# Performance work log

Measured on AMD Instinct MI355X. Metric: run time of the kernel, lower is better.

Reference implementation:

```python
import jax, jax.numpy as jnp
import numpy as np

N_NODES = 100000
N_EDGES = 1600000
D_INPUT = 128
D_HIDDEN = 16
N_HEADS = 8
NCLASSES = 40
N_GRAPHS = 64
ALPHA = 0.2  # LeakyReLU negative slope
INIT = 0.01  # GAT_param_init uniform range


def setup_inputs() -> dict:
    key = jax.random.key(0)
    ks = jax.random.split(key, 7)
    x = jax.random.normal(ks[0], (N_NODES, D_INPUT), dtype=jnp.float32)
    edge_idx = jax.random.randint(ks[1], (2, N_EDGES), 0, N_NODES, dtype=jnp.int64)
    batch = jnp.sort(jax.random.randint(ks[2], (N_NODES,), 0, N_GRAPHS, dtype=jnp.int64))
    # layer1: d_input -> n_heads * d_hidden, concat aggregate
    W1 = jax.random.uniform(ks[3], (D_INPUT, N_HEADS * D_HIDDEN), dtype=jnp.float32, minval=-INIT, maxval=INIT)
    a1 = jax.random.uniform(ks[4], (N_HEADS, 2 * D_HIDDEN), dtype=jnp.float32, minval=-INIT, maxval=INIT)
    # layer2: n_heads*d_hidden -> nclasses, 1 head, mean aggregate
    W2 = jax.random.uniform(ks[5], (N_HEADS * D_HIDDEN, NCLASSES), dtype=jnp.float32, minval=-INIT, maxval=INIT)
    a2 = jax.random.uniform(ks[6], (1, 2 * NCLASSES), dtype=jnp.float32, minval=-INIT, maxval=INIT)
    return {"x": x, "W1": W1, "a1": a1, "W2": W2, "a2": a2, "edge_idx": edge_idx, "batch": batch}


def _gat_layer(x, W, a, n_heads, d_out, src, dst, aggregate):
    # x: [N, d_in]; W: [d_in, H*D]; a: [H, 2*D]
    n = x.shape[0]
    Wh = (x @ W).reshape(n, n_heads, d_out)                  # [N, H, D]
    e_src = jnp.einsum('nhd,hd->nh', Wh, a[:, :d_out])       # [N, H]
    e_dst = jnp.einsum('nhd,hd->nh', Wh, a[:, d_out:])       # [N, H]
    e = jax.nn.leaky_relu(e_src[src] + e_dst[dst], ALPHA)    # [E, H]
    # segment softmax over edges sharing the same destination node
    m = jax.ops.segment_max(e, dst, num_segments=n)          # [N, H]
    m = jnp.where(jnp.isfinite(m), m, 0.0)                   # nodes w/o in-edges
    ex = jnp.exp(e - m[dst])
    s = jax.ops.segment_sum(ex, dst, num_segments=n)
    att = ex / (s[dst] + 1e-16)                              # [E, H]
    # weighted scatter-aggregate of neighbor features
    out = jax.ops.segment_sum(att[:, :, None] * Wh[src], dst, num_segments=n)  # [N, H, D]
    if aggregate == 'concat':
        return out.reshape(n, n_heads * d_out)
    return out.mean(axis=1)


def reference(x, W1, a1, W2, a2, edge_idx, batch):
    # eval mode: F.dropout(training=False) is identity
    src, dst = edge_idx[0], edge_idx[1]
    h1 = _gat_layer(x, W1, a1, N_HEADS, D_HIDDEN, src, dst, 'concat')
    h1 = jax.nn.elu(h1)
    h2 = _gat_layer(h1, W2, a2, 1, NCLASSES, src, dst, 'mean')   # [N, nclasses]
    # global_mean_pool over graph ids
    sums = jax.ops.segment_sum(h2, batch, num_segments=N_GRAPHS)
    cnt = jax.ops.segment_sum(jnp.ones((h2.shape[0],), h2.dtype), batch, num_segments=N_GRAPHS)
    return sums / jnp.maximum(cnt, 1.0)[:, None]
```

## Files before the change

### kernel.cpp

```cpp
#include <hip/hip_runtime.h>
#include <hip/hip_bf16.h>

typedef unsigned short u16;
typedef unsigned int   u32;

static constexpr int NN = 100000;
static constexpr int NE = 1600000;
static constexpr int NG = 64;

static constexpr int BSH   = 8;
static constexpr int NBUCK = 391;
static constexpr int BCAP  = 5120;
static constexpr int PB    = 8;

__device__ __forceinline__ u32 bf16pair(float a, float b) {
  u32 ua = __builtin_bit_cast(u32, a), ub = __builtin_bit_cast(u32, b);
  ua = (ua + 0x7FFFu + ((ua >> 16) & 1u)) >> 16;
  ub = (ub + 0x7FFFu + ((ub >> 16) & 1u)) >> 16;
  return ua | (ub << 16);
}
__device__ __forceinline__ float bflo(u32 u) { return __builtin_bit_cast(float, u << 16); }
__device__ __forceinline__ float bfhi(u32 u) { return __builtin_bit_cast(float, u & 0xFFFF0000u); }

__global__ __launch_bounds__(256) void k_gemm1(
    const float* __restrict__ x, const float* __restrict__ W1,
    const float* __restrict__ a1,
    u16* __restrict__ Wh1b, float* __restrict__ es1, float* __restrict__ ed1)
{
  __shared__ float xs[64][36];
  __shared__ float ws[32][128];
  const int t = threadIdx.x;
  const int rowBase = blockIdx.x * 64;
  const int r0 = (t >> 4) * 4;
  const int c0 = (t & 15) * 8;
  float acc[4][8];
#pragma unroll
  for (int r = 0; r < 4; ++r)
#pragma unroll
    for (int c = 0; c < 8; ++c) acc[r][c] = 0.f;

  for (int k0 = 0; k0 < 128; k0 += 32) {
#pragma unroll
    for (int p = 0; p < 2; ++p) {
      int rr = (t >> 3) + p * 32;
      int cc = (t & 7) * 4;
      int grow = rowBase + rr;
      float4 v = make_float4(0.f, 0.f, 0.f, 0.f);
      if (grow < NN) v = *(const float4*)(&x[(size_t)grow * 128 + k0 + cc]);
      *(float4*)(&xs[rr][cc]) = v;
    }
#pragma unroll
    for (int p = 0; p < 4; ++p) {
      int idx = (p * 256 + t) * 4;
      int kk = idx >> 7, cc = idx & 127;
      *(float4*)(&ws[kk][cc]) = *(const float4*)(&W1[(size_t)(k0 + kk) * 128 + cc]);
    }
    __syncthreads();
#pragma unroll
    for (int k = 0; k < 32; ++k) {
      float a[4], b[8];
#pragma unroll
      for (int r = 0; r < 4; ++r) a[r] = xs[r0 + r][k];
      *(float4*)&b[0] = *(float4*)&ws[k][c0];
      *(float4*)&b[4] = *(float4*)&ws[k][c0 + 4];
#pragma unroll
      for (int r = 0; r < 4; ++r)
#pragma unroll
        for (int c = 0; c < 8; ++c) acc[r][c] = fmaf(a[r], b[c], acc[r][c]);
    }
    __syncthreads();
  }
  const int h = (t & 15) >> 1;
  const int dbase = (t & 1) * 8;
  float a1s[8], a1d[8];
#pragma unroll
  for (int j = 0; j < 8; ++j) {
    a1s[j] = a1[h * 32 + dbase + j];
    a1d[j] = a1[h * 32 + 16 + dbase + j];
  }
#pragma unroll
  for (int r = 0; r < 4; ++r) {
    int grow = rowBase + r0 + r;
    float pes = 0.f, ped = 0.f;
#pragma unroll
    for (int j = 0; j < 8; ++j) {
      pes = fmaf(acc[r][j], a1s[j], pes);
      ped = fmaf(acc[r][j], a1d[j], ped);
    }
    pes += __shfl_xor(pes, 1);
    ped += __shfl_xor(ped, 1);
    if (grow < NN) {
      u32 p0 = bf16pair(acc[r][0], acc[r][1]);
      u32 p1 = bf16pair(acc[r][2], acc[r][3]);
      u32 p2 = bf16pair(acc[r][4], acc[r][5]);
      u32 p3 = bf16pair(acc[r][6], acc[r][7]);
      *(uint4*)(Wh1b + (size_t)grow * 128 + c0) = make_uint4(p0, p1, p2, p3);
      if ((t & 1) == 0) { es1[grow * 8 + h] = pes; ed1[grow * 8 + h] = ped; }
    }
  }
}

__global__ __launch_bounds__(256) void k_gemm2(
    const float* __restrict__ h1, const float* __restrict__ W2,
    const float* __restrict__ a2,
    u16* __restrict__ Wh2b, float* __restrict__ es2, float* __restrict__ ed2)
{
  __shared__ float hs[128][36];
  __shared__ float w2s[32][40];
  const int t = threadIdx.x;
  const int rowBase = blockIdx.x * 128;
  const int cg = t & 3;
  const int rs = t >> 2;
  float acc[2][10];
#pragma unroll
  for (int r = 0; r < 2; ++r)
#pragma unroll
    for (int j = 0; j < 10; ++j) acc[r][j] = 0.f;

  for (int k0 = 0; k0 < 128; k0 += 32) {
#pragma unroll
    for (int p = 0; p < 4; ++p) {
      int idx = (p * 256 + t) * 4;
      int rr = idx >> 5, cc = idx & 31;
      int grow = rowBase + rr;
      float4 v = make_float4(0.f, 0.f, 0.f, 0.f);
      if (grow < NN) v = *(const float4*)(&h1[(size_t)grow * 128 + k0 + cc]);
      *(float4*)(&hs[rr][cc]) = v;
    }
#pragma unroll
    for (int p = 0; p < 5; ++p) {
      int idx = p * 256 + t;
      int kk = idx / 40, cc = idx % 40;
      w2s[kk][cc] = W2[(size_t)(k0 + kk) * 40 + cc];
    }
    __syncthreads();
#pragma unroll
    for (int k = 0; k < 32; ++k) {
      float a0 = hs[rs][k], a1v = hs[rs + 64][k];
#pragma unroll
      for (int j = 0; j < 10; ++j) {
        float b = w2s[k][cg * 10 + j];
        acc[0][j] = fmaf(a0, b, acc[0][j]);
        acc[1][j] = fmaf(a1v, b, acc[1][j]);
      }
    }
    __syncthreads();
  }
  float a2s[10], a2d[10];
#pragma unroll
  for (int j = 0; j < 10; ++j) {
    a2s[j] = a2[cg * 10 + j];
    a2d[j] = a2[40 + cg * 10 + j];
  }
#pragma unroll
  for (int rr = 0; rr < 2; ++rr) {
    int grow = rowBase + rs + rr * 64;
    float pes = 0.f, ped = 0.f;
#pragma unroll
    for (int j = 0; j < 10; ++j) {
      float v = acc[rr][j];
      pes = fmaf(v, a2s[j], pes);
      ped = fmaf(v, a2d[j], ped);
    }
    if (grow < NN) {
      u32* dst = (u32*)(Wh2b + (size_t)grow * 48 + cg * 10);
      dst[0] = bf16pair(acc[rr][0], acc[rr][1]);
      dst[1] = bf16pair(acc[rr][2], acc[rr][3]);
      dst[2] = bf16pair(acc[rr][4], acc[rr][5]);
      dst[3] = bf16pair(acc[rr][6], acc[rr][7]);
      dst[4] = bf16pair(acc[rr][8], acc[rr][9]);
    }
    pes += __shfl_xor(pes, 1); pes += __shfl_xor(pes, 2);
    ped += __shfl_xor(ped, 1); ped += __shfl_xor(ped, 2);
    if (cg == 0 && grow < NN) { es2[grow] = pes; ed2[grow] = ped; }
  }
}

__global__ void k_initcur(int* __restrict__ cur) {
  int t = blockIdx.x * 256 + threadIdx.x;
  if (t < NBUCK) cur[t] = t * BCAP;
}

__global__ __launch_bounds__(256) void k_bin(
    const int* __restrict__ src, const int* __restrict__ dst,
    int* __restrict__ cur, u32* __restrict__ ebuf)
{
  __shared__ int lcnt[512];
  __shared__ int goff[NBUCK];
  __shared__ u32 bin[4096];
  const int t = threadIdx.x;
  const int e0 = blockIdx.x * 4096;

  lcnt[t] = 0; lcnt[t + 256] = 0;
  __syncthreads();

  u32 ent[16]; short bb[16], lp[16];
#pragma unroll
  for (int i = 0; i < 16; ++i) {
    int e = e0 + i * 256 + t;
    if (e < NE) {
      int s = src[e], d = dst[e];
      int b = d >> BSH;
      ent[i] = (u32)s | ((u32)(d & 255) << 20);
      bb[i] = (short)b;
      lp[i] = (short)atomicAdd(&lcnt[b], 1);
    } else bb[i] = -1;
  }
  __syncthreads();
  for (int d = 1; d < 512; d <<= 1) {
    int v0 = (t >= d) ? lcnt[t - d] : 0;
    int v1 = (t + 256 >= d) ? lcnt[t + 256 - d] : 0;
    __syncthreads();
    lcnt[t] += v0; lcnt[t + 256] += v1;
    __syncthreads();
  }
  for (int b = t; b < NBUCK; b += 256) {
    int excl = b ? lcnt[b - 1] : 0;
    int cnt = lcnt[b] - excl;
    if (cnt) goff[b] = atomicAdd(&cur[b], cnt);
  }
#pragma unroll
  for (int i = 0; i < 16; ++i) {
    if (bb[i] >= 0) {
      int excl = bb[i] ? lcnt[bb[i] - 1] : 0;
      bin[excl + lp[i]] = ent[i];
    }
  }
  __syncthreads();
  const int total = lcnt[NBUCK - 1];
  for (int i = t; i < total; i += 256) {
    int lo = 0, hi = NBUCK - 1;
    while (lo < hi) { int mid = (lo + hi) >> 1; if (lcnt[mid] > i) hi = mid; else lo = mid + 1; }
    int excl = lo ? lcnt[lo - 1] : 0;
    int g = goff[lo] + (i - excl);
    if (g < (lo + 1) * BCAP) ebuf[g] = bin[i];
  }
}

__global__ __launch_bounds__(256) void k_sort(
    const int* __restrict__ cur, u32* __restrict__ ebuf,
    int* __restrict__ offs, int* __restrict__ deg)
{
  __shared__ u32 ein[BCAP];
  __shared__ u32 eout[BCAP];
  __shared__ int nd[256];
  __shared__ int ncur[256];
  const int t = threadIdx.x;
  const int b = blockIdx.x;
  const int base = b * BCAP;
  int cnt = cur[b] - base;
  if (cnt > BCAP) cnt = BCAP;
  const int nloc = min(256, NN - (b << BSH));

  for (int i = t; i < cnt; i += 256) ein[i] = ebuf[base + i];
  nd[t] = 0;
  __syncthreads();
  for (int i = t; i < cnt; i += 256) atomicAdd(&nd[ein[i] >> 20], 1);
  __syncthreads();
  const int myCnt = nd[t];
  for (int d = 1; d < 256; d <<= 1) {
    int v = (t >= d) ? nd[t - d] : 0;
    __syncthreads();
    nd[t] += v;
    __syncthreads();
  }
  const int excl = t ? nd[t - 1] : 0;
  ncur[t] = excl;
  if (t < nloc) {
    int node = (b << BSH) + t;
    offs[node] = base + excl;
    deg[node]  = myCnt;
  }
  __syncthreads();
  for (int i = t; i < cnt; i += 256) {
    u32 v = ein[i];
    int pos = atomicAdd(&ncur[v >> 20], 1);
    eout[pos] = v & 0xFFFFFu;
  }
  __syncthreads();
  for (int i = t; i < cnt; i += 256) ebuf[base + i] = eout[i];
}

__global__ __launch_bounds__(256) void k_agg1(
    const u16* __restrict__ Wh1b, const float* __restrict__ es1, const float* __restrict__ ed1,
    const int* __restrict__ offs, const int* __restrict__ deg, const int* __restrict__ csr,
    float* __restrict__ h1)
{
  const int wid = threadIdx.x >> 6;
  const int lane = threadIdx.x & 63;
  const int n = blockIdx.x * 4 + wid;
  if (n >= NN) return;
  const int s0 = offs[n];
  const int nE = deg[n];
  const int g = lane >> 4;
  const int db = lane & 15;
  const int h = db >> 1;
  const float edv = ed1[n * 8 + h];

  float acc[8];
#pragma unroll
  for (int i = 0; i < 8; ++i) acc[i] = 0.f;
  float ssum = 0.f;

  for (int c0 = 0; c0 < nE; c0 += 8) {
    const int j0 = c0 + g;
    const int j1 = c0 + 4 + g;
    const int sA = csr[s0 + (j0 < nE ? j0 : 0)];
    const int sB = csr[s0 + (j1 < nE ? j1 : 0)];
    float zA = es1[sA * 8 + h] + edv;
    float zB = es1[sB * 8 + h] + edv;
    zA = (zA > 0.f) ? zA : 0.2f * zA;
    zB = (zB > 0.f) ? zB : 0.2f * zB;
    if (j0 < nE) {
      const uint4 raw = *(const uint4*)(Wh1b + (size_t)sA * 128 + db * 8);
      const float w = __expf(zA);
      ssum += w;
      acc[0] = fmaf(w, bflo(raw.x), acc[0]);
      acc[1] = fmaf(w, bfhi(raw.x), acc[1]);
      acc[2] = fmaf(w, bflo(raw.y), acc[2]);
      acc[3] = fmaf(w, bfhi(raw.y), acc[3]);
      acc[4] = fmaf(w, bflo(raw.z), acc[4]);
      acc[5] = fmaf(w, bfhi(raw.z), acc[5]);
      acc[6] = fmaf(w, bflo(raw.w), acc[6]);
      acc[7] = fmaf(w, bfhi(raw.w), acc[7]);
    }
    if (j1 < nE) {
      const uint4 raw = *(const uint4*)(Wh1b + (size_t)sB * 128 + db * 8);
      const float w = __expf(zB);
      ssum += w;
      acc[0] = fmaf(w, bflo(raw.x), acc[0]);
      acc[1] = fmaf(w, bfhi(raw.x), acc[1]);
      acc[2] = fmaf(w, bflo(raw.y), acc[2]);
      acc[3] = fmaf(w, bfhi(raw.y), acc[3]);
      acc[4] = fmaf(w, bflo(raw.z), acc[4]);
      acc[5] = fmaf(w, bfhi(raw.z), acc[5]);
      acc[6] = fmaf(w, bflo(raw.w), acc[6]);
      acc[7] = fmaf(w, bfhi(raw.w), acc[7]);
    }
  }
#pragma unroll
  for (int i = 0; i < 8; ++i) {
    acc[i] += __shfl_xor(acc[i], 16);
    acc[i] += __shfl_xor(acc[i], 32);
  }
  ssum += __shfl_xor(ssum, 16);
  ssum += __shfl_xor(ssum, 32);

  if (g == 0) {
    float inv = 1.f / (ssum + 1e-16f);
    float o[8];
#pragma unroll
    for (int i = 0; i < 8; ++i) {
      float v = acc[i] * inv;
      o[i] = (v > 0.f) ? v : expm1f(v);
    }
    float* dst = h1 + (size_t)n * 128 + db * 8;
    *(float4*)(dst)     = make_float4(o[0], o[1], o[2], o[3]);
    *(float4*)(dst + 4) = make_float4(o[4], o[5], o[6], o[7]);
  }
}

__global__ __launch_bounds__(256) void k_agg2(
    const u16* __restrict__ Wh2b, const float* __restrict__ es2, const float* __restrict__ ed2,
    const int* __restrict__ offs, const int* __restrict__ deg, const int* __restrict__ csr,
    float* __restrict__ h2)
{
  __shared__ float red[4][64][9];
  const int wid = threadIdx.x >> 6;
  const int lane = threadIdx.x & 63;
  const int n = blockIdx.x * 4 + wid;
  if (n >= NN) return;
  const int s0 = offs[n];
  const int nE = deg[n];
  const float edv = ed2[n];
  const int e5 = lane / 5, r5 = lane - e5 * 5;
  const bool act = lane < 60;

  float acc[8];
#pragma unroll
  for (int i = 0; i < 8; ++i) acc[i] = 0.f;
  float ssum = 0.f;

  for (int c0 = 0; c0 < nE; c0 += 24) {
    const int j0 = c0 + e5;
    const int j1 = c0 + 12 + e5;
    const int sA = csr[s0 + (j0 < nE ? j0 : 0)];
    const int sB = csr[s0 + (j1 < nE ? j1 : 0)];
    float zA = es2[sA] + edv;
    float zB = es2[sB] + edv;
    zA = (zA > 0.f) ? zA : 0.2f * zA;
    zB = (zB > 0.f) ? zB : 0.2f * zB;
    if (act && j0 < nE) {
      const uint4 raw = *(const uint4*)(Wh2b + (size_t)sA * 48 + r5 * 8);
      const float w = __expf(zA);
      ssum += w;
      acc[0] = fmaf(w, bflo(raw.x), acc[0]);
      acc[1] = fmaf(w, bfhi(raw.x), acc[1]);
      acc[2] = fmaf(w, bflo(raw.y), acc[2]);
      acc[3] = fmaf(w, bfhi(raw.y), acc[3]);
      acc[4] = fmaf(w, bflo(raw.z), acc[4]);
      acc[5] = fmaf(w, bfhi(raw.z), acc[5]);
      acc[6] = fmaf(w, bflo(raw.w), acc[6]);
      acc[7] = fmaf(w, bfhi(raw.w), acc[7]);
    }
    if (act && j1 < nE) {
      const uint4 raw = *(const uint4*)(Wh2b + (size_t)sB * 48 + r5 * 8);
      const float w = __expf(zB);
      ssum += w;
      acc[0] = fmaf(w, bflo(raw.x), acc[0]);
      acc[1] = fmaf(w, bfhi(raw.x), acc[1]);
      acc[2] = fmaf(w, bflo(raw.y), acc[2]);
      acc[3] = fmaf(w, bfhi(raw.y), acc[3]);
      acc[4] = fmaf(w, bflo(raw.z), acc[4]);
      acc[5] = fmaf(w, bfhi(raw.z), acc[5]);
      acc[6] = fmaf(w, bflo(raw.w), acc[6]);
      acc[7] = fmaf(w, bfhi(raw.w), acc[7]);
    }
  }
#pragma unroll
  for (int i = 0; i < 8; ++i) red[wid][lane][i] = acc[i];
  red[wid][lane][8] = ssum;
  __builtin_amdgcn_wave_barrier();
  if (lane < 40) {
    int slot = lane >> 3, i = lane & 7;
    float a = 0.f, sm = 0.f;
#pragma unroll
    for (int g = 0; g < 12; ++g) {
      a  += red[wid][g * 5 + slot][i];
      sm += red[wid][g * 5][8];
    }
    h2[(size_t)n * 40 + lane] = a / (sm + 1e-16f);
  }
}

__global__ void k_gbounds(const int* __restrict__ batch, int* __restrict__ gstart) {
  int g = threadIdx.x;
  if (g > NG) return;
  int lo = 0, hi = NN;
  while (lo < hi) { int mid = (lo + hi) >> 1; if (batch[mid] < g) lo = mid + 1; else hi = mid; }
  gstart[g] = lo;
}

__global__ __launch_bounds__(256) void k_pool1(
    const float* __restrict__ h2, const int* __restrict__ gstart,
    float* __restrict__ partial)
{
  __shared__ float lds[25][10][4];
  const int g = blockIdx.x >> 3;
  const int p = blockIdx.x & 7;
  const int t = threadIdx.x;
  const int s0 = gstart[g], s1 = gstart[g + 1];
  const int len = s1 - s0;
  const int chunk = (len + PB - 1) / PB;
  const int start = s0 + p * chunk;
  const int end = min(start + chunk, s1);
  const int slot = t / 10, q = t - slot * 10;
  float4 acc = make_float4(0.f, 0.f, 0.f, 0.f);
  if (slot < 25) {
    for (int n = start + slot; n < end; n += 25) {
      const float4 v = *(const float4*)(&h2[(size_t)n * 40 + q * 4]);
      acc.x += v.x; acc.y += v.y; acc.z += v.z; acc.w += v.w;
    }
    lds[slot][q][0] = acc.x; lds[slot][q][1] = acc.y;
    lds[slot][q][2] = acc.z; lds[slot][q][3] = acc.w;
  }
  __syncthreads();
  if (t < 40) {
    const int qq = t >> 2, e = t & 3;
    float s = 0.f;
#pragma unroll
    for (int sl = 0; sl < 25; ++sl) s += lds[sl][qq][e];
    partial[(size_t)blockIdx.x * 40 + t] = s;
  }
}

__global__ void k_pool2(const float* __restrict__ partial, const int* __restrict__ gstart,
                        float* __restrict__ out)
{
  const int g = blockIdx.x;
  const int d = threadIdx.x;
  if (d >= 40) return;
  float s = 0.f;
#pragma unroll
  for (int p = 0; p < PB; ++p) s += partial[(size_t)(g * PB + p) * 40 + d];
  int cnt = gstart[g + 1] - gstart[g];
  if (cnt < 1) cnt = 1;
  out[g * 40 + d] = s / (float)cnt;
}

extern "C" void kernel_launch(void* const* d_in, const int* in_sizes, int n_in,
                              void* d_out, int out_size, void* d_ws, size_t ws_size,
                              hipStream_t stream)
{
  const float* x   = (const float*)d_in[0];
  const float* W1  = (const float*)d_in[1];
  const float* a1  = (const float*)d_in[2];
  const float* W2  = (const float*)d_in[3];
  const float* a2  = (const float*)d_in[4];
  const int* eidx  = (const int*)d_in[5];
  const int* batch = (const int*)d_in[6];
  float* out = (float*)d_out;

  char* ws = (char*)d_ws;
  u16*   Wh1b = (u16*)(ws + 0);
  u16*   Wh2b = (u16*)(ws + 0);
  float* h2   = (float*)(ws + 9600000);
  float* h1   = (float*)(ws + 25600000);
  float* es1  = (float*)(ws + 76800000);
  float* ed1  = (float*)(ws + 80000000);
  float* es2  = (float*)(ws + 83200000);
  float* ed2  = (float*)(ws + 83600000);
  u32*   ebuf = (u32*)(ws + 84000000);
  int*   offs = (int*)(ws + 92007680);
  int*   deg  = (int*)(ws + 92407680);
  int*   cur  = (int*)(ws + 92807680);
  int*   gstart = (int*)(ws + 92809728);
  float* partial = (float*)(ws + 92810240);

  const int* esrc = eidx;
  const int* edst = eidx + NE;

  k_initcur<<<2, 256, 0, stream>>>(cur);
  k_gbounds<<<1, 128, 0, stream>>>(batch, gstart);
  k_gemm1<<<(NN + 63) / 64, 256, 0, stream>>>(x, W1, a1, Wh1b, es1, ed1);
  k_bin<<<(NE + 4095) / 4096, 256, 0, stream>>>(esrc, edst, cur, ebuf);
  k_sort<<<NBUCK, 256, 0, stream>>>(cur, ebuf, offs, deg);
  k_agg1<<<(NN + 3) / 4, 256, 0, stream>>>(Wh1b, es1, ed1, offs, deg, (const int*)ebuf, h1);
  k_gemm2<<<(NN + 127) / 128, 256, 0, stream>>>(h1, W2, a2, Wh2b, es2, ed2);
  k_agg2<<<(NN + 3) / 4, 256, 0, stream>>>(Wh2b, es2, ed2, offs, deg, (const int*)ebuf, h2);
  k_pool1<<<NG * PB, 256, 0, stream>>>(h2, gstart, partial);
  k_pool2<<<NG, 64, 0, stream>>>(partial, gstart, out);
}
```

Before: 284.0 us.

## Fuse front kernels, store h1 in bf16, use packed FMA in aggregations

Merges edge binning, the first GEMM and the graph-bound search into one launch with a shared-memory union, and replaces the cursor-init kernel with a memset by making bucket cursors relative. Layer-1 output is now written as bf16 and converted back to fp32 inside the second GEMM, halving that intermediate traffic. Both aggregation kernels switch to v_pk_fma_f32 inline asm on float2 accumulators to halve FMA issue count. The bf16 h1 adds rounding error into layer 2, and the inline asm constrains compiler scheduling.

```diff
diff --git a/kernel.cpp b/kernel.cpp
--- a/kernel.cpp
+++ b/kernel.cpp
@@ -3,6 +3,7 @@
 
 typedef unsigned short u16;
 typedef unsigned int   u32;
+typedef float f32x2 __attribute__((ext_vector_type(2)));
 
 static constexpr int NN = 100000;
 static constexpr int NE = 1600000;
@@ -12,6 +13,7 @@
 static constexpr int NBUCK = 391;
 static constexpr int BCAP  = 5120;
 static constexpr int PB    = 8;
+static constexpr int NB_G1 = (NN + 63) / 64;
 
 __device__ __forceinline__ u32 bf16pair(float a, float b) {
   u32 ua = __builtin_bit_cast(u32, a), ub = __builtin_bit_cast(u32, b);
@@ -22,15 +24,84 @@
 __device__ __forceinline__ float bflo(u32 u) { return __builtin_bit_cast(float, u << 16); }
 __device__ __forceinline__ float bfhi(u32 u) { return __builtin_bit_cast(float, u & 0xFFFF0000u); }
 
-__global__ __launch_bounds__(256) void k_gemm1(
-    const float* __restrict__ x, const float* __restrict__ W1,
-    const float* __restrict__ a1,
-    u16* __restrict__ Wh1b, float* __restrict__ es1, float* __restrict__ ed1)
-{
-  __shared__ float xs[64][36];
-  __shared__ float ws[32][128];
+__device__ __forceinline__ void pkfma(f32x2& a, f32x2 w2, u32 u) {
+  f32x2 v;
+  v.x = bflo(u); v.y = bfhi(u);
+  asm("v_pk_fma_f32 %0, %1, %2, %0" : "+v"(a) : "v"(w2), "v"(v));
+}
+
+__global__ __launch_bounds__(256) void k_front(
+    const float* __restrict__ x, const float* __restrict__ W1, const float* __restrict__ a1,
+    const int* __restrict__ esrc, const int* __restrict__ edst, const int* __restrict__ batch,
+    u16* __restrict__ Wh1b, float* __restrict__ es1, float* __restrict__ ed1,
+    int* __restrict__ cur, u32* __restrict__ ebuf, int* __restrict__ gstart)
+{
+  __shared__ union U {
+    struct { float xs[64][36]; float ws[32][128]; } g;
+    struct { int lcnt[512]; int goff[NBUCK]; u32 bin[4096]; } b;
+  } sm;
+  const int bid = blockIdx.x;
   const int t = threadIdx.x;
-  const int rowBase = blockIdx.x * 64;
+
+  if (bid < NBUCK) {
+    const int e0 = bid * 4096;
+    sm.b.lcnt[t] = 0; sm.b.lcnt[t + 256] = 0;
+    __syncthreads();
+    u32 ent[16]; short bb[16], lp[16];
+#pragma unroll
+    for (int i = 0; i < 16; ++i) {
+      int e = e0 + i * 256 + t;
+      if (e < NE) {
+        int s = esrc[e], d = edst[e];
+        int b = d >> BSH;
+        ent[i] = (u32)s | ((u32)(d & 255) << 20);
+        bb[i] = (short)b;
+        lp[i] = (short)atomicAdd(&sm.b.lcnt[b], 1);
+      } else bb[i] = -1;
+    }
+    __syncthreads();
+    for (int d = 1; d < 512; d <<= 1) {
+      int v0 = (t >= d) ? sm.b.lcnt[t - d] : 0;
+      int v1 = (t + 256 >= d) ? sm.b.lcnt[t + 256 - d] : 0;
+      __syncthreads();
+      sm.b.lcnt[t] += v0; sm.b.lcnt[t + 256] += v1;
+      __syncthreads();
+    }
+    for (int b = t; b < NBUCK; b += 256) {
+      int excl = b ? sm.b.lcnt[b - 1] : 0;
+      int cnt = sm.b.lcnt[b] - excl;
+      if (cnt) sm.b.goff[b] = b * BCAP + atomicAdd(&cur[b], cnt);
+    }
+#pragma unroll
+    for (int i = 0; i < 16; ++i) {
+      if (bb[i] >= 0) {
+        int excl = bb[i] ? sm.b.lcnt[bb[i] - 1] : 0;
+        sm.b.bin[excl + lp[i]] = ent[i];
+      }
+    }
+    __syncthreads();
+    const int total = sm.b.lcnt[NBUCK - 1];
+    for (int i = t; i < total; i += 256) {
+      int lo = 0, hi = NBUCK - 1;
+      while (lo < hi) { int mid = (lo + hi) >> 1; if (sm.b.lcnt[mid] > i) hi = mid; else lo = mid + 1; }
+      int excl = lo ? sm.b.lcnt[lo - 1] : 0;
+      int g = sm.b.goff[lo] + (i - excl);
+      if (g < (lo + 1) * BCAP) ebuf[g] = sm.b.bin[i];
+    }
+    return;
+  }
+
+  if (bid == NBUCK + NB_G1) {
+    int g = t;
+    if (g <= NG) {
+      int lo = 0, hi = NN;
+      while (lo < hi) { int mid = (lo + hi) >> 1; if (batch[mid] < g) lo = mid + 1; else hi = mid; }
+      gstart[g] = lo;
+    }
+    return;
+  }
+
+  const int rowBase = (bid - NBUCK) * 64;
   const int r0 = (t >> 4) * 4;
   const int c0 = (t & 15) * 8;
   float acc[4][8];
@@ -47,22 +118,22 @@
       int grow = rowBase + rr;
       float4 v = make_float4(0.f, 0.f, 0.f, 0.f);
       if (grow < NN) v = *(const float4*)(&x[(size_t)grow * 128 + k0 + cc]);
-      *(float4*)(&xs[rr][cc]) = v;
+      *(float4*)(&sm.g.xs[rr][cc]) = v;
     }
 #pragma unroll
     for (int p = 0; p < 4; ++p) {
       int idx = (p * 256 + t) * 4;
       int kk = idx >> 7, cc = idx & 127;
-      *(float4*)(&ws[kk][cc]) = *(const float4*)(&W1[(size_t)(k0 + kk) * 128 + cc]);
+      *(float4*)(&sm.g.ws[kk][cc]) = *(const float4*)(&W1[(size_t)(k0 + kk) * 128 + cc]);
     }
     __syncthreads();
 #pragma unroll
     for (int k = 0; k < 32; ++k) {
       float a[4], b[8];
 #pragma unroll
-      for (int r = 0; r < 4; ++r) a[r] = xs[r0 + r][k];
-      *(float4*)&b[0] = *(float4*)&ws[k][c0];
-      *(float4*)&b[4] = *(float4*)&ws[k][c0 + 4];
+      for (int r = 0; r < 4; ++r) a[r] = sm.g.xs[r0 + r][k];
+      *(float4*)&b[0] = *(float4*)&sm.g.ws[k][c0];
+      *(float4*)&b[4] = *(float4*)&sm.g.ws[k][c0 + 4];
 #pragma unroll
       for (int r = 0; r < 4; ++r)
 #pragma unroll
@@ -100,143 +171,6 @@
   }
 }
 
-__global__ __launch_bounds__(256) void k_gemm2(
-    const float* __restrict__ h1, const float* __restrict__ W2,
-    const float* __restrict__ a2,
-    u16* __restrict__ Wh2b, float* __restrict__ es2, float* __restrict__ ed2)
-{
-  __shared__ float hs[128][36];
-  __shared__ float w2s[32][40];
-  const int t = threadIdx.x;
-  const int rowBase = blockIdx.x * 128;
-  const int cg = t & 3;
-  const int rs = t >> 2;
-  float acc[2][10];
-#pragma unroll
-  for (int r = 0; r < 2; ++r)
-#pragma unroll
-    for (int j = 0; j < 10; ++j) acc[r][j] = 0.f;
-
-  for (int k0 = 0; k0 < 128; k0 += 32) {
-#pragma unroll
-    for (int p = 0; p < 4; ++p) {
-      int idx = (p * 256 + t) * 4;
-      int rr = idx >> 5, cc = idx & 31;
-      int grow = rowBase + rr;
-      float4 v = make_float4(0.f, 0.f, 0.f, 0.f);
-      if (grow < NN) v = *(const float4*)(&h1[(size_t)grow * 128 + k0 + cc]);
-      *(float4*)(&hs[rr][cc]) = v;
-    }
-#pragma unroll
-    for (int p = 0; p < 5; ++p) {
-      int idx = p * 256 + t;
-      int kk = idx / 40, cc = idx % 40;
-      w2s[kk][cc] = W2[(size_t)(k0 + kk) * 40 + cc];
-    }
-    __syncthreads();
-#pragma unroll
-    for (int k = 0; k < 32; ++k) {
-      float a0 = hs[rs][k], a1v = hs[rs + 64][k];
-#pragma unroll
-      for (int j = 0; j < 10; ++j) {
-        float b = w2s[k][cg * 10 + j];
-        acc[0][j] = fmaf(a0, b, acc[0][j]);
-        acc[1][j] = fmaf(a1v, b, acc[1][j]);
-      }
-    }
-    __syncthreads();
-  }
-  float a2s[10], a2d[10];
-#pragma unroll
-  for (int j = 0; j < 10; ++j) {
-    a2s[j] = a2[cg * 10 + j];
-    a2d[j] = a2[40 + cg * 10 + j];
-  }
-#pragma unroll
-  for (int rr = 0; rr < 2; ++rr) {
-    int grow = rowBase + rs + rr * 64;
-    float pes = 0.f, ped = 0.f;
-#pragma unroll
-    for (int j = 0; j < 10; ++j) {
-      float v = acc[rr][j];
-      pes = fmaf(v, a2s[j], pes);
-      ped = fmaf(v, a2d[j], ped);
-    }
-    if (grow < NN) {
-      u32* dst = (u32*)(Wh2b + (size_t)grow * 48 + cg * 10);
-      dst[0] = bf16pair(acc[rr][0], acc[rr][1]);
-      dst[1] = bf16pair(acc[rr][2], acc[rr][3]);
-      dst[2] = bf16pair(acc[rr][4], acc[rr][5]);
-      dst[3] = bf16pair(acc[rr][6], acc[rr][7]);
-      dst[4] = bf16pair(acc[rr][8], acc[rr][9]);
-    }
-    pes += __shfl_xor(pes, 1); pes += __shfl_xor(pes, 2);
-    ped += __shfl_xor(ped, 1); ped += __shfl_xor(ped, 2);
-    if (cg == 0 && grow < NN) { es2[grow] = pes; ed2[grow] = ped; }
-  }
-}
-
-__global__ void k_initcur(int* __restrict__ cur) {
-  int t = blockIdx.x * 256 + threadIdx.x;
-  if (t < NBUCK) cur[t] = t * BCAP;
-}
-
-__global__ __launch_bounds__(256) void k_bin(
-    const int* __restrict__ src, const int* __restrict__ dst,
-    int* __restrict__ cur, u32* __restrict__ ebuf)
-{
-  __shared__ int lcnt[512];
-  __shared__ int goff[NBUCK];
-  __shared__ u32 bin[4096];
-  const int t = threadIdx.x;
-  const int e0 = blockIdx.x * 4096;
-
-  lcnt[t] = 0; lcnt[t + 256] = 0;
-  __syncthreads();
-
-  u32 ent[16]; short bb[16], lp[16];
-#pragma unroll
-  for (int i = 0; i < 16; ++i) {
-    int e = e0 + i * 256 + t;
-    if (e < NE) {
-      int s = src[e], d = dst[e];
-      int b = d >> BSH;
-      ent[i] = (u32)s | ((u32)(d & 255) << 20);
-      bb[i] = (short)b;
-      lp[i] = (short)atomicAdd(&lcnt[b], 1);
-    } else bb[i] = -1;
-  }
-  __syncthreads();
-  for (int d = 1; d < 512; d <<= 1) {
-    int v0 = (t >= d) ? lcnt[t - d] : 0;
-    int v1 = (t + 256 >= d) ? lcnt[t + 256 - d] : 0;
-    __syncthreads();
-    lcnt[t] += v0; lcnt[t + 256] += v1;
-    __syncthreads();
-  }
-  for (int b = t; b < NBUCK; b += 256) {
-    int excl = b ? lcnt[b - 1] : 0;
-    int cnt = lcnt[b] - excl;
-    if (cnt) goff[b] = atomicAdd(&cur[b], cnt);
-  }
-#pragma unroll
-  for (int i = 0; i < 16; ++i) {
-    if (bb[i] >= 0) {
-      int excl = bb[i] ? lcnt[bb[i] - 1] : 0;
-      bin[excl + lp[i]] = ent[i];
-    }
-  }
-  __syncthreads();
-  const int total = lcnt[NBUCK - 1];
-  for (int i = t; i < total; i += 256) {
-    int lo = 0, hi = NBUCK - 1;
-    while (lo < hi) { int mid = (lo + hi) >> 1; if (lcnt[mid] > i) hi = mid; else lo = mid + 1; }
-    int excl = lo ? lcnt[lo - 1] : 0;
-    int g = goff[lo] + (i - excl);
-    if (g < (lo + 1) * BCAP) ebuf[g] = bin[i];
-  }
-}
-
 __global__ __launch_bounds__(256) void k_sort(
     const int* __restrict__ cur, u32* __restrict__ ebuf,
     int* __restrict__ offs, int* __restrict__ deg)
@@ -248,7 +182,7 @@
   const int t = threadIdx.x;
   const int b = blockIdx.x;
   const int base = b * BCAP;
-  int cnt = cur[b] - base;
+  int cnt = cur[b];
   if (cnt > BCAP) cnt = BCAP;
   const int nloc = min(256, NN - (b << BSH));
 
@@ -284,7 +218,7 @@
 __global__ __launch_bounds__(256) void k_agg1(
     const u16* __restrict__ Wh1b, const float* __restrict__ es1, const float* __restrict__ ed1,
     const int* __restrict__ offs, const int* __restrict__ deg, const int* __restrict__ csr,
-    float* __restrict__ h1)
+    u16* __restrict__ h1b)
 {
   const int wid = threadIdx.x >> 6;
   const int lane = threadIdx.x & 63;
@@ -297,9 +231,9 @@
   const int h = db >> 1;
   const float edv = ed1[n * 8 + h];
 
-  float acc[8];
-#pragma unroll
-  for (int i = 0; i < 8; ++i) acc[i] = 0.f;
+  f32x2 acc[4];
+#pragma unroll
+  for (int i = 0; i < 4; ++i) { acc[i].x = 0.f; acc[i].y = 0.f; }
   float ssum = 0.f;
 
   for (int c0 = 0; c0 < nE; c0 += 8) {
@@ -315,33 +249,29 @@
       const uint4 raw = *(const uint4*)(Wh1b + (size_t)sA * 128 + db * 8);
       const float w = __expf(zA);
       ssum += w;
-      acc[0] = fmaf(w, bflo(raw.x), acc[0]);
-      acc[1] = fmaf(w, bfhi(raw.x), acc[1]);
-      acc[2] = fmaf(w, bflo(raw.y), acc[2]);
-      acc[3] = fmaf(w, bfhi(raw.y), acc[3]);
-      acc[4] = fmaf(w, bflo(raw.z), acc[4]);
-      acc[5] = fmaf(w, bfhi(raw.z), acc[5]);
-      acc[6] = fmaf(w, bflo(raw.w), acc[6]);
-      acc[7] = fmaf(w, bfhi(raw.w), acc[7]);
+      f32x2 w2; w2.x = w; w2.y = w;
+      pkfma(acc[0], w2, raw.x);
+      pkfma(acc[1], w2, raw.y);
+      pkfma(acc[2], w2, raw.z);
+      pkfma(acc[3], w2, raw.w);
     }
     if (j1 < nE) {
       const uint4 raw = *(const uint4*)(Wh1b + (size_t)sB * 128 + db * 8);
       const float w = __expf(zB);
       ssum += w;
-      acc[0] = fmaf(w, bflo(raw.x), acc[0]);
-      acc[1] = fmaf(w, bfhi(raw.x), acc[1]);
-      acc[2] = fmaf(w, bflo(raw.y), acc[2]);
-      acc[3] = fmaf(w, bfhi(raw.y), acc[3]);
-      acc[4] = fmaf(w, bflo(raw.z), acc[4]);
-      acc[5] = fmaf(w, bfhi(raw.z), acc[5]);
-      acc[6] = fmaf(w, bflo(raw.w), acc[6]);
-      acc[7] = fmaf(w, bfhi(raw.w), acc[7]);
-    }
-  }
-#pragma unroll
-  for (int i = 0; i < 8; ++i) {
-    acc[i] += __shfl_xor(acc[i], 16);
-    acc[i] += __shfl_xor(acc[i], 32);
+      f32x2 w2; w2.x = w; w2.y = w;
+      pkfma(acc[0], w2, raw.x);
+      pkfma(acc[1], w2, raw.y);
+      pkfma(acc[2], w2, raw.z);
+      pkfma(acc[3], w2, raw.w);
+    }
+  }
+#pragma unroll
+  for (int i = 0; i < 4; ++i) {
+    acc[i].x += __shfl_xor(acc[i].x, 16);
+    acc[i].y += __shfl_xor(acc[i].y, 16);
+    acc[i].x += __shfl_xor(acc[i].x, 32);
+    acc[i].y += __shfl_xor(acc[i].y, 32);
   }
   ssum += __shfl_xor(ssum, 16);
   ssum += __shfl_xor(ssum, 32);
@@ -350,13 +280,97 @@
     float inv = 1.f / (ssum + 1e-16f);
     float o[8];
 #pragma unroll
-    for (int i = 0; i < 8; ++i) {
-      float v = acc[i] * inv;
-      o[i] = (v > 0.f) ? v : expm1f(v);
-    }
-    float* dst = h1 + (size_t)n * 128 + db * 8;
-    *(float4*)(dst)     = make_float4(o[0], o[1], o[2], o[3]);
-    *(float4*)(dst + 4) = make_float4(o[4], o[5], o[6], o[7]);
+    for (int i = 0; i < 4; ++i) {
+      float v0 = acc[i].x * inv;
+      float v1 = acc[i].y * inv;
+      o[2 * i]     = (v0 > 0.f) ? v0 : expm1f(v0);
+      o[2 * i + 1] = (v1 > 0.f) ? v1 : expm1f(v1);
+    }
+    u32 p0 = bf16pair(o[0], o[1]);
+    u32 p1 = bf16pair(o[2], o[3]);
+    u32 p2 = bf16pair(o[4], o[5]);
+    u32 p3 = bf16pair(o[6], o[7]);
+    *(uint4*)(h1b + (size_t)n * 128 + db * 8) = make_uint4(p0, p1, p2, p3);
+  }
+}
+
+__global__ __launch_bounds__(256) void k_gemm2(
+    const u16* __restrict__ h1b, const float* __restrict__ W2,
+    const float* __restrict__ a2,
+    u16* __restrict__ Wh2b, float* __restrict__ es2, float* __restrict__ ed2)
+{
+  __shared__ float hs[128][36];
+  __shared__ float w2s[32][40];
+  const int t = threadIdx.x;
+  const int rowBase = blockIdx.x * 128;
+  const int cg = t & 3;
+  const int rs = t >> 2;
+  float acc[2][10];
+#pragma unroll
+  for (int r = 0; r < 2; ++r)
+#pragma unroll
+    for (int j = 0; j < 10; ++j) acc[r][j] = 0.f;
+
+  for (int k0 = 0; k0 < 128; k0 += 32) {
+#pragma unroll
+    for (int p = 0; p < 2; ++p) {
+      int idx = (p * 256 + t) * 8;
+      int rr = idx >> 5, cc = idx & 31;
+      int grow = rowBase + rr;
+      uint4 hv = make_uint4(0u, 0u, 0u, 0u);
+      if (grow < NN) hv = *(const uint4*)(h1b + (size_t)grow * 128 + k0 + cc);
+      float2* dst = (float2*)&hs[rr][cc];
+      dst[0] = make_float2(bflo(hv.x), bfhi(hv.x));
+      dst[1] = make_float2(bflo(hv.y), bfhi(hv.y));
+      dst[2] = make_float2(bflo(hv.z), bfhi(hv.z));
+      dst[3] = make_float2(bflo(hv.w), bfhi(hv.w));
+    }
+#pragma unroll
+    for (int p = 0; p < 5; ++p) {
+      int idx = p * 256 + t;
+      int kk = idx / 40, cc = idx % 40;
+      w2s[kk][cc] = W2[(size_t)(k0 + kk) * 40 + cc];
+    }
+    __syncthreads();
+#pragma unroll
+    for (int k = 0; k < 32; ++k) {
+      float a0 = hs[rs][k], a1v = hs[rs + 64][k];
+#pragma unroll
+      for (int j = 0; j < 10; ++j) {
+        float b = w2s[k][cg * 10 + j];
+        acc[0][j] = fmaf(a0, b, acc[0][j]);
+        acc[1][j] = fmaf(a1v, b, acc[1][j]);
+      }
+    }
+    __syncthreads();
+  }
+  float a2s[10], a2d[10];
+#pragma unroll
+  for (int j = 0; j < 10; ++j) {
+    a2s[j] = a2[cg * 10 + j];
+    a2d[j] = a2[40 + cg * 10 + j];
+  }
+#pragma unroll
+  for (int rr = 0; rr < 2; ++rr) {
+    int grow = rowBase + rs + rr * 64;
+    float pes = 0.f, ped = 0.f;
+#pragma unroll
+    for (int j = 0; j < 10; ++j) {
+      float v = acc[rr][j];
+      pes = fmaf(v, a2s[j], pes);
+      ped = fmaf(v, a2d[j], ped);
+    }
+    if (grow < NN) {
+      u32* dst = (u32*)(Wh2b + (size_t)grow * 48 + cg * 10);
+      dst[0] = bf16pair(acc[rr][0], acc[rr][1]);
+      dst[1] = bf16pair(acc[rr][2], acc[rr][3]);
+      dst[2] = bf16pair(acc[rr][4], acc[rr][5]);
+      dst[3] = bf16pair(acc[rr][6], acc[rr][7]);
+      dst[4] = bf16pair(acc[rr][8], acc[rr][9]);
+    }
+    pes += __shfl_xor(pes, 1); pes += __shfl_xor(pes, 2);
+    ped += __shfl_xor(ped, 1); ped += __shfl_xor(ped, 2);
+    if (cg == 0 && grow < NN) { es2[grow] = pes; ed2[grow] = ped; }
   }
 }
 
@@ -376,9 +390,9 @@
   const int e5 = lane / 5, r5 = lane - e5 * 5;
   const bool act = lane < 60;
 
-  float acc[8];
-#pragma unroll
-  for (int i = 0; i < 8; ++i) acc[i] = 0.f;
+  f32x2 acc[4];
+#pragma unroll
+  for (int i = 0; i < 4; ++i) { acc[i].x = 0.f; acc[i].y = 0.f; }
   float ssum = 0.f;
 
   for (int c0 = 0; c0 < nE; c0 += 24) {
@@ -394,31 +408,28 @@
       const uint4 raw = *(const uint4*)(Wh2b + (size_t)sA * 48 + r5 * 8);
       const float w = __expf(zA);
       ssum += w;
-      acc[0] = fmaf(w, bflo(raw.x), acc[0]);
-      acc[1] = fmaf(w, bfhi(raw.x), acc[1]);
-      acc[2] = fmaf(w, bflo(raw.y), acc[2]);
-      acc[3] = fmaf(w, bfhi(raw.y), acc[3]);
-      acc[4] = fmaf(w, bflo(raw.z), acc[4]);
-      acc[5] = fmaf(w, bfhi(raw.z), acc[5]);
-      acc[6] = fmaf(w, bflo(raw.w), acc[6]);
-      acc[7] = fmaf(w, bfhi(raw.w), acc[7]);
+      f32x2 w2; w2.x = w; w2.y = w;
+      pkfma(acc[0], w2, raw.x);
+      pkfma(acc[1], w2, raw.y);
+      pkfma(acc[2], w2, raw.z);
+      pkfma(acc[3], w2, raw.w);
     }
     if (act && j1 < nE) {
       const uint4 raw = *(const uint4*)(Wh2b + (size_t)sB * 48 + r5 * 8);
       const float w = __expf(zB);
       ssum += w;
-      acc[0] = fmaf(w, bflo(raw.x), acc[0]);
-      acc[1] = fmaf(w, bfhi(raw.x), acc[1]);
-      acc[2] = fmaf(w, bflo(raw.y), acc[2]);
-      acc[3] = fmaf(w, bfhi(raw.y), acc[3]);
-      acc[4] = fmaf(w, bflo(raw.z), acc[4]);
-      acc[5] = fmaf(w, bfhi(raw.z), acc[5]);
-      acc[6] = fmaf(w, bflo(raw.w), acc[6]);
-      acc[7] = fmaf(w, bfhi(raw.w), acc[7]);
-    }
-  }
-#pragma unroll
-  for (int i = 0; i < 8; ++i) red[wid][lane][i] = acc[i];
+      f32x2 w2; w2.x = w; w2.y = w;
+      pkfma(acc[0], w2, raw.x);
+      pkfma(acc[1], w2, raw.y);
+      pkfma(acc[2], w2, raw.z);
+      pkfma(acc[3], w2, raw.w);
+    }
+  }
+#pragma unroll
+  for (int i = 0; i < 4; ++i) {
+    red[wid][lane][2 * i]     = acc[i].x;
+    red[wid][lane][2 * i + 1] = acc[i].y;
+  }
   red[wid][lane][8] = ssum;
   __builtin_amdgcn_wave_barrier();
   if (lane < 40) {
@@ -431,14 +442,6 @@
     }
     h2[(size_t)n * 40 + lane] = a / (sm + 1e-16f);
   }
-}
-
-__global__ void k_gbounds(const int* __restrict__ batch, int* __restrict__ gstart) {
-  int g = threadIdx.x;
-  if (g > NG) return;
-  int lo = 0, hi = NN;
-  while (lo < hi) { int mid = (lo + hi) >> 1; if (batch[mid] < g) lo = mid + 1; else hi = mid; }
-  gstart[g] = lo;
 }
 
 __global__ __launch_bounds__(256) void k_pool1(
@@ -505,28 +508,27 @@
   u16*   Wh1b = (u16*)(ws + 0);
   u16*   Wh2b = (u16*)(ws + 0);
   float* h2   = (float*)(ws + 9600000);
-  float* h1   = (float*)(ws + 25600000);
-  float* es1  = (float*)(ws + 76800000);
-  float* ed1  = (float*)(ws + 80000000);
-  float* es2  = (float*)(ws + 83200000);
-  float* ed2  = (float*)(ws + 83600000);
-  u32*   ebuf = (u32*)(ws + 84000000);
-  int*   offs = (int*)(ws + 92007680);
-  int*   deg  = (int*)(ws + 92407680);
-  int*   cur  = (int*)(ws + 92807680);
-  int*   gstart = (int*)(ws + 92809728);
-  float* partial = (float*)(ws + 92810240);
+  u16*   h1b  = (u16*)(ws + 25600000);
+  float* es1  = (float*)(ws + 51200000);
+  float* ed1  = (float*)(ws + 54400000);
+  float* es2  = (float*)(ws + 57600000);
+  float* ed2  = (float*)(ws + 58000000);
+  u32*   ebuf = (u32*)(ws + 58400000);
+  int*   offs = (int*)(ws + 66407680);
+  int*   deg  = (int*)(ws + 66807680);
+  int*   cur  = (int*)(ws + 67207680);
+  int*   gstart = (int*)(ws + 67209728);
+  float* partial = (float*)(ws + 67210240);
 
   const int* esrc = eidx;
   const int* edst = eidx + NE;
 
-  k_initcur<<<2, 256, 0, stream>>>(cur);
-  k_gbounds<<<1, 128, 0, stream>>>(batch, gstart);
-  k_gemm1<<<(NN + 63) / 64, 256, 0, stream>>>(x, W1, a1, Wh1b, es1, ed1);
-  k_bin<<<(NE + 4095) / 4096, 256, 0, stream>>>(esrc, edst, cur, ebuf);
+  hipMemsetAsync(cur, 0, NBUCK * sizeof(int), stream);
+  k_front<<<NBUCK + NB_G1 + 1, 256, 0, stream>>>(x, W1, a1, esrc, edst, batch,
+                                                 Wh1b, es1, ed1, cur, ebuf, gstart);
   k_sort<<<NBUCK, 256, 0, stream>>>(cur, ebuf, offs, deg);
-  k_agg1<<<(NN + 3) / 4, 256, 0, stream>>>(Wh1b, es1, ed1, offs, deg, (const int*)ebuf, h1);
-  k_gemm2<<<(NN + 127) / 128, 256, 0, stream>>>(h1, W2, a2, Wh2b, es2, ed2);
+  k_agg1<<<(NN + 3) / 4, 256, 0, stream>>>(Wh1b, es1, ed1, offs, deg, (const int*)ebuf, h1b);
+  k_gemm2<<<(NN + 127) / 128, 256, 0, stream>>>(h1b, W2, a2, Wh2b, es2, ed2);
   k_agg2<<<(NN + 3) / 4, 256, 0, stream>>>(Wh2b, es2, ed2, offs, deg, (const int*)ebuf, h2);
   k_pool1<<<NG * PB, 256, 0, stream>>>(h2, gstart, partial);
   k_pool2<<<NG, 64, 0, stream>>>(partial, gstart, out);
```

Result: slower. 388.1 us (+36.7%).
